# Performance work log

Measured on AMD Instinct MI355X. Metric: run time of the kernel, lower is better.

The kernel has to match this reference:

```python
import jax, jax.numpy as jnp
from jax import lax
import numpy as np

SCALE_N = 4
KERN = 5
PAD = KERN // 2
_G = np.float32([[0.003765, 0.015019, 0.023792, 0.015019, 0.003765],
                 [0.015019, 0.059912, 0.094907, 0.059912, 0.015019],
                 [0.023792, 0.094907, 0.150342, 0.094907, 0.023792],
                 [0.015019, 0.059912, 0.094907, 0.059912, 0.015019],
                 [0.003765, 0.015019, 0.023792, 0.015019, 0.003765]])
FILTER = jnp.asarray(_G)


def _lap_split(img):
    N, c, H, W = img.shape
    f = jnp.broadcast_to(FILTER, (c, 1, KERN, KERN))
    smooth = lax.conv_general_dilated(img, f, (1, 1), [(PAD, PAD), (PAD, PAD)],
                                      feature_group_count=c)
    lo = smooth[:, :, ::2, ::2]
    oph, opw = (H + 1) % 2, (W + 1) % 2
    # conv_transpose2d(stride=2, padding=PAD, output_padding) as lhs-dilated conv
    # (Gaussian kernel is symmetric, so no spatial flip needed)
    lo2 = 4.0 * lax.conv_general_dilated(
        lo, f, (1, 1),
        [(KERN - 1 - PAD, KERN - 1 - PAD + oph), (KERN - 1 - PAD, KERN - 1 - PAD + opw)],
        lhs_dilation=(2, 2), feature_group_count=c)
    hi = img - lo2
    return lo, hi


def _pyramid(img):
    levels = []
    for _ in range(SCALE_N):
        img, hi = _lap_split(img)
        levels.append(hi)
    levels.append(img)
    return levels


def _sample_points(img, xs, ys):
    # bilinear grid_sample, align_corners=False, zero padding.
    # img: (N,C,H,W); xs, ys: (P,) normalized coords in [-1,1]. -> (N,C,P)
    N, C, H, W = img.shape
    fx = ((xs + 1.0) * W - 1.0) * 0.5
    fy = ((ys + 1.0) * H - 1.0) * 0.5
    x0 = jnp.floor(fx)
    y0 = jnp.floor(fy)
    wx = fx - x0
    wy = fy - y0
    x0i = x0.astype(jnp.int32)
    y0i = y0.astype(jnp.int32)
    out = jnp.zeros((N, C, xs.shape[0]), img.dtype)
    corners = [(0, 0, (1 - wx) * (1 - wy)), (1, 0, wx * (1 - wy)),
               (0, 1, (1 - wx) * wy), (1, 1, wx * wy)]
    for dx, dy, w in corners:
        xc = x0i + dx
        yc = y0i + dy
        valid = (xc >= 0) & (xc < W) & (yc >= 0) & (yc < H)
        xcc = jnp.clip(xc, 0, W - 1)
        ycc = jnp.clip(yc, 0, H - 1)
        vals = img[:, :, ycc, xcc]  # (N,C,P) gather
        out = out + vals * (w * valid)[None, None, :]
    return out


def setup_inputs() -> dict:
    key = jax.random.key(0)
    k1, k2, k3 = jax.random.split(key, 3)
    N, c, H, W = 64, 32, 128, 128
    outdims = 4096
    m = SCALE_N + 1
    x = jax.random.normal(k1, (N, c, H, W), dtype=jnp.float32)
    grid = jax.random.uniform(k2, (1, outdims, 1, 2), minval=-0.1, maxval=0.1,
                              dtype=jnp.float32)
    features = (jnp.full((1, m * c, 1, outdims), 1.0 / c, jnp.float32)
                + 0.01 * jax.random.normal(k3, (1, m * c, 1, outdims), jnp.float32))
    bias = jnp.zeros((outdims,), jnp.float32)
    return {"x": x, "grid": grid, "features": features, "bias": bias}


def reference(x, grid, features, bias):
    N, c, H, W = x.shape
    m = SCALE_N + 1
    outdims = grid.shape[1]
    g = jnp.clip(grid, -1.0, 1.0)
    xs = g[0, :, 0, 0]  # width coord
    ys = g[0, :, 0, 1]  # height coord
    levels = _pyramid(x)
    pools = [_sample_points(lv, xs, ys) for lv in levels]  # each (N,c,P)
    y = jnp.concatenate(pools, axis=1)  # (N, m*c, P)
    feat = features.reshape(1, m * c, outdims)
    y = (y * feat).sum(axis=1)  # (N, P)
    return y + bias
```

## Files before the change

### kernel.cpp

```cpp
#include <hip/hip_runtime.h>


#define P1 66
#define P2 34
#define P3 18
#define P4 10
#define OFF_LO1 0
#define OFF_LO2 4224
#define OFF_LO3 5312
#define OFF_LO4 5600
#define SLOT    5680

#define G_A 0.0613609f
#define G_B 0.2447700f
#define G_C 0.3877386f

static __device__ __forceinline__ float clampf(float v, float lo, float hi) {
    return fminf(fmaxf(v, lo), hi);
}
static __device__ __forceinline__ int imin(int a, int b) { return a < b ? a : b; }
static __device__ __forceinline__ int imax(int a, int b) { return a > b ? a : b; }

__global__ void init_out_kernel(const float* __restrict__ bias, float* __restrict__ y) {
    int i = blockIdx.x * blockDim.x + threadIdx.x;
    y[i] = bias[i & 4095];
}

__global__ void weights_kernel(const float* __restrict__ grid, float* __restrict__ ws) {
    int out = blockIdx.x * blockDim.x + threadIdx.x;
    if (out >= 4096) return;
    float xs = clampf(grid[2 * out + 0], -1.f, 1.f);
    float ys = clampf(grid[2 * out + 1], -1.f, 1.f);
    float rec[88];

    float fx = (xs + 1.f) * 64.f - 0.5f;
    float fy = (ys + 1.f) * 64.f - 0.5f;
    float x0f = floorf(fx), y0f = floorf(fy);
    int x0 = (int)x0f, y0 = (int)y0f;
    float wx = fx - x0f, wy = fy - y0f;
    float ux0 = (x0 >= 0)      ? (1.f - wx) : 0.f;
    float ux1 = (x0 + 1 < 128) ? wx         : 0.f;
    float uy0 = (y0 >= 0)      ? (1.f - wy) : 0.f;
    float uy1 = (y0 + 1 < 128) ? wy         : 0.f;
    int cx0 = imax(x0, 0), cx1 = imin(x0 + 1, 127);
    int cy0 = imax(y0, 0), cy1 = imin(y0 + 1, 127);
    rec[0] = ux0 * uy0; rec[1] = ux1 * uy0; rec[2] = ux0 * uy1; rec[3] = ux1 * uy1;
    rec[4] = __int_as_float(cy0 * 128 + cx0);
    rec[5] = __int_as_float(cy0 * 128 + cx1);
    rec[6] = __int_as_float(cy1 * 128 + cx0);
    rec[7] = __int_as_float(cy1 * 128 + cx1);

    int   x0p = x0, y0p = y0;
    float ux0p = ux0, ux1p = ux1, uy0p = uy0, uy1p = uy1;

    const int offs[4]    = {OFF_LO1, OFF_LO2, OFF_LO3, OFF_LO4};
    const int strides[4] = {P1, P2, P3, P4};

    for (int j = 1; j <= 4; ++j) {
        const int Wj = 128 >> j, Pj = strides[j - 1], off = offs[j - 1];

        int qx; float a0, a1, a2;
        if (x0p & 1) { qx = (x0p - 1) >> 1;
            a0 = G_B * ux0p + G_A * ux1p; a1 = G_B * ux0p + G_C * ux1p; a2 = G_A * ux1p; }
        else         { qx = (x0p >> 1) - 1;
            a0 = G_A * ux0p; a1 = G_C * ux0p + G_B * ux1p; a2 = G_A * ux0p + G_B * ux1p; }
        int qy; float e0, e1, e2;
        if (y0p & 1) { qy = (y0p - 1) >> 1;
            e0 = G_B * uy0p + G_A * uy1p; e1 = G_B * uy0p + G_C * uy1p; e2 = G_A * uy1p; }
        else         { qy = (y0p >> 1) - 1;
            e0 = G_A * uy0p; e1 = G_C * uy0p + G_B * uy1p; e2 = G_A * uy0p + G_B * uy1p; }

        float half = (float)(Wj >> 1);
        float fxj = (xs + 1.f) * half - 0.5f;
        float fyj = (ys + 1.f) * half - 0.5f;
        float x0jf = floorf(fxj), y0jf = floorf(fyj);
        int x0j = (int)x0jf, y0j = (int)y0jf;
        float wxj = fxj - x0jf, wyj = fyj - y0jf;
        float ux0j = (x0j >= 0)     ? (1.f - wxj) : 0.f;
        float ux1j = (x0j + 1 < Wj) ? wxj         : 0.f;
        float uy0j = (y0j >= 0)     ? (1.f - wyj) : 0.f;
        float uy1j = (y0j + 1 < Wj) ? wyj         : 0.f;

        int bxb = qx & ~1;
        bxb = imin(imax(bxb, 0), Wj - 4);

        float* L = rec + 8 + (j - 1) * 20;
#pragma unroll
        for (int t = 0; t < 4; ++t) {
            int col = bxb + t;
            int s = col - qx;
            float av = (s == 0) ? a0 : (s == 1) ? a1 : (s == 2) ? a2 : 0.f;
            if (s < 0 || s > 2) av = 0.f;
            int sb = col - x0j;
            float bv = (sb == 0) ? ux0j : (sb == 1) ? ux1j : 0.f;
            L[t] = av;
            L[4 + t] = bv;
        }
#pragma unroll
        for (int t = 0; t < 3; ++t) {
            int row = qy + t;
            bool v = (row >= 0) && (row < Wj);
            float av = (t == 0) ? e0 : (t == 1) ? e1 : e2;
            L[8 + t] = v ? av : 0.f;
            int sb = row - y0j;
            L[12 + t] = (sb == 0) ? uy0j : (sb == 1) ? uy1j : 0.f;
            int rc = imin(imax(row, 0), Wj - 1);
            L[16 + t] = __int_as_float(off + rc * Pj + bxb);
        }
        L[11] = 0.f; L[15] = 0.f; L[19] = 0.f;

        x0p = x0j; y0p = y0j;
        ux0p = ux0j; ux1p = ux1j; uy0p = uy0j; uy1p = uy1j;
    }

    float4* W = (float4*)ws;
#pragma unroll
    for (int m = 0; m < 22; ++m) {
        W[m * 4096 + out] = make_float4(rec[4 * m], rec[4 * m + 1],
                                        rec[4 * m + 2], rec[4 * m + 3]);
    }
}

static __device__ __forceinline__ float down_pt_lds(const float* s, int stride, int S,
                                                    int i, int j) {
    const float g1[5] = {G_A, G_B, G_C, G_B, G_A};
    int by = 2 * i - 2, bx = 2 * j - 2;
    float acc = 0.f;
    if (by >= 0 && by + 4 < S && bx >= 0 && bx + 4 < S) {
#pragma unroll
        for (int dy = 0; dy < 5; ++dy) {
            const float* r = s + (by + dy) * stride + bx;
            acc += g1[dy] * (G_A * (r[0] + r[4]) + G_B * (r[1] + r[3]) + G_C * r[2]);
        }
    } else {
#pragma unroll
        for (int dy = 0; dy < 5; ++dy) {
            int yy = by + dy;
            if ((unsigned)yy < (unsigned)S) {
#pragma unroll
                for (int dx = 0; dx < 5; ++dx) {
                    int xx = bx + dx;
                    if ((unsigned)xx < (unsigned)S)
                        acc += g1[dy] * g1[dx] * s[yy * stride + xx];
                }
            }
        }
    }
    return acc;
}

__global__ __launch_bounds__(256, 3) void pyr_sample_kernel(
    const float* __restrict__ x, const float* __restrict__ wrec,
    const float* __restrict__ feat, float* __restrict__ y)
{
    __shared__ float s_lo[SLOT];
    const int tid = threadIdx.x;
    const int n   = blockIdx.x >> 5;
    const int c   = blockIdx.x & 31;
    const float* img = x + ((size_t)(n * 32 + c) << 14);

    const float g1[5] = {G_A, G_B, G_C, G_B, G_A};

    for (int r = tid; r < 1024; r += 256) {
        int i = r >> 4, j0 = (r & 15) << 2;
        int by = 2 * i - 2, bx = 2 * j0 - 2;
        float acc[4] = {0.f, 0.f, 0.f, 0.f};
        if (i >= 1 && i <= 62 && j0 >= 4 && j0 <= 56) {
#pragma unroll
            for (int dy = 0; dy < 5; ++dy) {
                const float* row = img + (by + dy) * 128 + bx;
                float v[11];
#pragma unroll
                for (int t = 0; t < 11; ++t) v[t] = row[t];
                float g = g1[dy];
#pragma unroll
                for (int jj = 0; jj < 4; ++jj) {
                    float h = G_A * (v[2 * jj] + v[2 * jj + 4]) +
                              G_B * (v[2 * jj + 1] + v[2 * jj + 3]) +
                              G_C * v[2 * jj + 2];
                    acc[jj] += g * h;
                }
            }
        } else {
#pragma unroll
            for (int dy = 0; dy < 5; ++dy) {
                int yy = by + dy;
                if ((unsigned)yy < 128u) {
#pragma unroll
                    for (int t = 0; t < 11; ++t) {
                        int xx = bx + t;
                        if ((unsigned)xx < 128u) {
                            float v = img[yy * 128 + xx];
#pragma unroll
                            for (int jj = 0; jj < 4; ++jj) {
                                int dx = t - 2 * jj;
                                if (dx >= 0 && dx <= 4) acc[jj] += g1[dy] * g1[dx] * v;
                            }
                        }
                    }
                }
            }
        }
        int base = OFF_LO1 + i * P1 + j0;
        *(float2*)&s_lo[base]     = make_float2(acc[0], acc[1]);
        *(float2*)&s_lo[base + 2] = make_float2(acc[2], acc[3]);
    }
    __syncthreads();

    for (int p = tid; p < 1024; p += 256) {
        int i = p >> 5, j = p & 31;
        s_lo[OFF_LO2 + i * P2 + j] = down_pt_lds(s_lo + OFF_LO1, P1, 64, i, j);
    }
    __syncthreads();

    {
        int i = tid >> 4, j = tid & 15;
        s_lo[OFF_LO3 + i * P3 + j] = down_pt_lds(s_lo + OFF_LO2, P2, 32, i, j);
    }
    __syncthreads();

    if (tid < 64) {
        int i = tid >> 3, j = tid & 7;
        s_lo[OFF_LO4 + i * P4 + j] = down_pt_lds(s_lo + OFF_LO3, P3, 16, i, j);
    }
    __syncthreads();

    const float4* W = (const float4*)wrec;
    float* yrow = y + ((size_t)n << 12);
    for (int out = tid; out < 4096; out += 256) {
        float4 w0 = W[out];
        float4 t1 = W[4096 + out];
        int o00 = __float_as_int(t1.x), o01 = __float_as_int(t1.y);
        int o10 = __float_as_int(t1.z), o11 = __float_as_int(t1.w);

        float f_prev = feat[((size_t)c << 12) + out];
        float v0 = w0.x * img[o00] + w0.y * img[o01] + w0.z * img[o10] + w0.w * img[o11];
        float acc = f_prev * v0;

#pragma unroll
        for (int j = 1; j <= 4; ++j) {
            const int mb = (2 + 5 * (j - 1)) * 4096 + out;
            const float4 axw = W[mb];
            const float4 bxw = W[mb + 4096];
            const float4 ayw = W[mb + 2 * 4096];
            const float4 byw = W[mb + 3 * 4096];
            const float4 rrf = W[mb + 4 * 4096];
            int r0 = __float_as_int(rrf.x);
            int r1 = __float_as_int(rrf.y);
            int r2 = __float_as_int(rrf.z);

            float f_cur = feat[((size_t)(j * 32 + c) << 12) + out];

            float2 p0a = *(const float2*)&s_lo[r0];
            float2 p0b = *(const float2*)&s_lo[r0 + 2];
            float2 p1a = *(const float2*)&s_lo[r1];
            float2 p1b = *(const float2*)&s_lo[r1 + 2];
            float2 p2a = *(const float2*)&s_lo[r2];
            float2 p2b = *(const float2*)&s_lo[r2 + 2];
            float ra0 = axw.x * p0a.x + axw.y * p0a.y + axw.z * p0b.x + axw.w * p0b.y;
            float ra1 = axw.x * p1a.x + axw.y * p1a.y + axw.z * p1b.x + axw.w * p1b.y;
            float ra2 = axw.x * p2a.x + axw.y * p2a.y + axw.z * p2b.x + axw.w * p2b.y;
            float rb0 = bxw.x * p0a.x + bxw.y * p0a.y + bxw.z * p0b.x + bxw.w * p0b.y;
            float rb1 = bxw.x * p1a.x + bxw.y * p1a.y + bxw.z * p1b.x + bxw.w * p1b.y;
            float rb2 = bxw.x * p2a.x + bxw.y * p2a.y + bxw.z * p2b.x + bxw.w * p2b.y;
            float sa = ayw.x * ra0 + ayw.y * ra1 + ayw.z * ra2;
            float sb = byw.x * rb0 + byw.y * rb1 + byw.z * rb2;
            acc += f_cur * sb - 4.f * f_prev * sa;
            f_prev = f_cur;
        }
        atomicAdd(&yrow[out], acc);
    }
}

extern "C" void kernel_launch(void* const* d_in, const int* in_sizes, int n_in,
                              void* d_out, int out_size, void* d_ws, size_t ws_size,
                              hipStream_t stream) {
    (void)in_sizes; (void)n_in; (void)ws_size;
    const float* x    = (const float*)d_in[0];
    const float* grid = (const float*)d_in[1];
    const float* feat = (const float*)d_in[2];
    const float* bias = (const float*)d_in[3];
    float* y  = (float*)d_out;
    float* ws = (float*)d_ws;

    weights_kernel<<<16, 256, 0, stream>>>(grid, ws);
    init_out_kernel<<<out_size / 256, 256, 0, stream>>>(bias, y);
    pyr_sample_kernel<<<2048, 256, 0, stream>>>(x, ws, feat, y);
}
```

Before: 403.7 us.

## Split pyramid build and sampling into two kernels, replacing atomics with block reduction

The fused per-(n,c) kernel becomes two kernels. The first builds the low-pass pyramid and writes it to workspace. The second tiles over (n, 64 outputs), stages the sampling weights in LDS, loops over channels, and reduces with a shared-memory sum instead of global atomicAdd. This removes the atomic contention and the bias-init kernel, and reuses the weight records across channels. In exchange the pyramid makes an extra round trip through global memory and pyramid taps are read from global instead of LDS. A fused fallback path remains for when the workspace is too small.

```diff
diff --git a/kernel.cpp b/kernel.cpp
--- a/kernel.cpp
+++ b/kernel.cpp
@@ -14,6 +14,10 @@
 #define G_A 0.0613609f
 #define G_B 0.2447700f
 #define G_C 0.3877386f
+
+#define W4COUNT (22 * 4096)
+#define PYR_OFF_FLOATS (W4COUNT * 4)
+#define WS_NEED ((size_t)PYR_OFF_FLOATS * 4 + (size_t)2048 * SLOT * 4)
 
 static __device__ __forceinline__ float clampf(float v, float lo, float hi) {
     return fminf(fmaxf(v, lo), hi);
@@ -115,10 +119,9 @@
 
     float4* W = (float4*)ws;
 #pragma unroll
-    for (int m = 0; m < 22; ++m) {
+    for (int m = 0; m < 22; ++m)
         W[m * 4096 + out] = make_float4(rec[4 * m], rec[4 * m + 1],
                                         rec[4 * m + 2], rec[4 * m + 3]);
-    }
 }
 
 static __device__ __forceinline__ float down_pt_lds(const float* s, int stride, int S,
@@ -149,16 +152,7 @@
     return acc;
 }
 
-__global__ __launch_bounds__(256, 3) void pyr_sample_kernel(
-    const float* __restrict__ x, const float* __restrict__ wrec,
-    const float* __restrict__ feat, float* __restrict__ y)
-{
-    __shared__ float s_lo[SLOT];
-    const int tid = threadIdx.x;
-    const int n   = blockIdx.x >> 5;
-    const int c   = blockIdx.x & 31;
-    const float* img = x + ((size_t)(n * 32 + c) << 14);
-
+static __device__ void build_pyramid(const float* __restrict__ img, float* s_lo, int tid) {
     const float g1[5] = {G_A, G_B, G_C, G_B, G_A};
 
     for (int r = tid; r < 1024; r += 256) {
@@ -224,6 +218,113 @@
         s_lo[OFF_LO4 + i * P4 + j] = down_pt_lds(s_lo + OFF_LO3, P3, 16, i, j);
     }
     __syncthreads();
+}
+
+__global__ __launch_bounds__(256, 3) void pyr_build_kernel(
+    const float* __restrict__ x, float* __restrict__ pyr)
+{
+    __shared__ __align__(16) float s_lo[SLOT];
+    const int tid = threadIdx.x;
+    const float* img = x + ((size_t)blockIdx.x << 14);
+    build_pyramid(img, s_lo, tid);
+    float4* dst = (float4*)(pyr + (size_t)blockIdx.x * SLOT);
+    const float4* src = (const float4*)s_lo;
+    for (int i = tid; i < SLOT / 4; i += 256) dst[i] = src[i];
+}
+
+__global__ __launch_bounds__(256, 3) void sample_kernel(
+    const float* __restrict__ x, const float* __restrict__ wrec,
+    const float* __restrict__ pyr, const float* __restrict__ feat,
+    const float* __restrict__ bias, float* __restrict__ y)
+{
+    __shared__ __align__(16) float4 Wl[22 * 64];
+    __shared__ float red[4][64];
+    const int tid = threadIdx.x;
+    const int n   = blockIdx.x >> 6;
+    const int o0  = (blockIdx.x & 63) << 6;
+
+    const float4* Wg = (const float4*)wrec;
+    for (int i = tid; i < 22 * 64; i += 256)
+        Wl[i] = Wg[(i >> 6) * 4096 + o0 + (i & 63)];
+    __syncthreads();
+
+    const int lane = tid & 63, q = tid >> 6;
+    const int out  = o0 + lane;
+    const float* xn = x + ((size_t)n << 19);
+    const float* pn = pyr + (size_t)(n << 5) * SLOT;
+
+    float4 w0 = Wl[lane];
+    float4 t1 = Wl[64 + lane];
+    int o00 = __float_as_int(t1.x), o01 = __float_as_int(t1.y);
+    int o10 = __float_as_int(t1.z), o11 = __float_as_int(t1.w);
+
+    float acc = 0.f;
+    float fprev[8];
+#pragma unroll 4
+    for (int i = 0; i < 8; ++i) {
+        const int c = q * 8 + i;
+        const float* img = xn + ((size_t)c << 14);
+        float f = feat[((size_t)c << 12) + out];
+        float v0 = w0.x * img[o00] + w0.y * img[o01] +
+                   w0.z * img[o10] + w0.w * img[o11];
+        acc += f * v0;
+        fprev[i] = f;
+    }
+
+#pragma unroll
+    for (int j = 1; j <= 4; ++j) {
+        const int mb = (2 + 5 * (j - 1)) * 64 + lane;
+        float4 axw = Wl[mb];
+        float4 bxw = Wl[mb + 64];
+        float4 ayw = Wl[mb + 128];
+        float4 byw = Wl[mb + 192];
+        float4 rrf = Wl[mb + 256];
+        int r0 = __float_as_int(rrf.x);
+        int r1 = __float_as_int(rrf.y);
+        int r2 = __float_as_int(rrf.z);
+
+#pragma unroll 4
+        for (int i = 0; i < 8; ++i) {
+            const int c = q * 8 + i;
+            const float* P = pn + (size_t)c * SLOT;
+            float2 p0a = *(const float2*)(P + r0);
+            float2 p0b = *(const float2*)(P + r0 + 2);
+            float2 p1a = *(const float2*)(P + r1);
+            float2 p1b = *(const float2*)(P + r1 + 2);
+            float2 p2a = *(const float2*)(P + r2);
+            float2 p2b = *(const float2*)(P + r2 + 2);
+            float f = feat[((size_t)(j * 32 + c) << 12) + out];
+            float ra0 = axw.x * p0a.x + axw.y * p0a.y + axw.z * p0b.x + axw.w * p0b.y;
+            float ra1 = axw.x * p1a.x + axw.y * p1a.y + axw.z * p1b.x + axw.w * p1b.y;
+            float ra2 = axw.x * p2a.x + axw.y * p2a.y + axw.z * p2b.x + axw.w * p2b.y;
+            float rb0 = bxw.x * p0a.x + bxw.y * p0a.y + bxw.z * p0b.x + bxw.w * p0b.y;
+            float rb1 = bxw.x * p1a.x + bxw.y * p1a.y + bxw.z * p1b.x + bxw.w * p1b.y;
+            float rb2 = bxw.x * p2a.x + bxw.y * p2a.y + bxw.z * p2b.x + bxw.w * p2b.y;
+            float sa = ayw.x * ra0 + ayw.y * ra1 + ayw.z * ra2;
+            float sb = byw.x * rb0 + byw.y * rb1 + byw.z * rb2;
+            acc += f * sb - 4.f * fprev[i] * sa;
+            fprev[i] = f;
+        }
+    }
+
+    red[q][lane] = acc;
+    __syncthreads();
+    if (tid < 64) {
+        float s = red[0][tid] + red[1][tid] + red[2][tid] + red[3][tid];
+        y[((size_t)n << 12) + o0 + tid] = s + bias[o0 + tid];
+    }
+}
+
+__global__ __launch_bounds__(256, 3) void fused_fallback_kernel(
+    const float* __restrict__ x, const float* __restrict__ wrec,
+    const float* __restrict__ feat, float* __restrict__ y)
+{
+    __shared__ __align__(16) float s_lo[SLOT];
+    const int tid = threadIdx.x;
+    const int n   = blockIdx.x >> 5;
+    const int c   = blockIdx.x & 31;
+    const float* img = x + ((size_t)(n * 32 + c) << 14);
+    build_pyramid(img, s_lo, tid);
 
     const float4* W = (const float4*)wrec;
     float* yrow = y + ((size_t)n << 12);
@@ -248,9 +349,7 @@
             int r0 = __float_as_int(rrf.x);
             int r1 = __float_as_int(rrf.y);
             int r2 = __float_as_int(rrf.z);
-
             float f_cur = feat[((size_t)(j * 32 + c) << 12) + out];
-
             float2 p0a = *(const float2*)&s_lo[r0];
             float2 p0b = *(const float2*)&s_lo[r0 + 2];
             float2 p1a = *(const float2*)&s_lo[r1];
@@ -275,7 +374,7 @@
 extern "C" void kernel_launch(void* const* d_in, const int* in_sizes, int n_in,
                               void* d_out, int out_size, void* d_ws, size_t ws_size,
                               hipStream_t stream) {
-    (void)in_sizes; (void)n_in; (void)ws_size;
+    (void)in_sizes; (void)n_in;
     const float* x    = (const float*)d_in[0];
     const float* grid = (const float*)d_in[1];
     const float* feat = (const float*)d_in[2];
@@ -284,6 +383,12 @@
     float* ws = (float*)d_ws;
 
     weights_kernel<<<16, 256, 0, stream>>>(grid, ws);
-    init_out_kernel<<<out_size / 256, 256, 0, stream>>>(bias, y);
-    pyr_sample_kernel<<<2048, 256, 0, stream>>>(x, ws, feat, y);
-}
+    if (ws_size >= WS_NEED) {
+        float* pyr = ws + PYR_OFF_FLOATS;
+        pyr_build_kernel<<<2048, 256, 0, stream>>>(x, pyr);
+        sample_kernel<<<4096, 256, 0, stream>>>(x, ws, pyr, feat, bias, y);
+    } else {
+        init_out_kernel<<<out_size / 256, 256, 0, stream>>>(bias, y);
+        fused_fallback_kernel<<<2048, 256, 0, stream>>>(x, ws, feat, y);
+    }
+}
```

After: 450.3 us. +11.6%, slower.

## Pack sampling weight records into fp16 weights and 16-bit indices; vectorize level-1 loads

Applied to the files above, without the earlier changes.

Sampling weights are stored as packed half-precision pairs and the LDS/image indices as 16-bit pairs, which shrinks the per-output weight table each block streams from global memory. The level-1 downsampling now loads each input row with four aligned float4 reads instead of eleven scalar loads. The aim is less memory traffic in the gather loop at the cost of unpack instructions and reduced weight precision, which may affect accuracy tolerance.

```diff
diff --git a/kernel.cpp b/kernel.cpp
--- a/kernel.cpp
+++ b/kernel.cpp
@@ -1,4 +1,5 @@
 #include <hip/hip_runtime.h>
+#include <hip/hip_fp16.h>
 
 
 #define P1 66
@@ -15,11 +16,27 @@
 #define G_B 0.2447700f
 #define G_C 0.3877386f
 
+#define T_FOFF 16384
+
 static __device__ __forceinline__ float clampf(float v, float lo, float hi) {
     return fminf(fmaxf(v, lo), hi);
 }
 static __device__ __forceinline__ int imin(int a, int b) { return a < b ? a : b; }
 static __device__ __forceinline__ int imax(int a, int b) { return a > b ? a : b; }
+
+static __device__ __forceinline__ unsigned int pack_h2(float a, float b) {
+    __half ha = __float2half_rn(a), hb = __float2half_rn(b);
+    unsigned short ua = *(unsigned short*)&ha, ub = *(unsigned short*)&hb;
+    return (unsigned int)ua | ((unsigned int)ub << 16);
+}
+static __device__ __forceinline__ unsigned int pack_u2(int a, int b) {
+    return (unsigned int)(a & 0xffff) | ((unsigned int)b << 16);
+}
+static __device__ __forceinline__ float2 uph2(unsigned int u) {
+    unsigned short lo = (unsigned short)(u & 0xffff), hi = (unsigned short)(u >> 16);
+    __half hl = *(__half*)&lo, hh = *(__half*)&hi;
+    return make_float2(__half2float(hl), __half2float(hh));
+}
 
 __global__ void init_out_kernel(const float* __restrict__ bias, float* __restrict__ y) {
     int i = blockIdx.x * blockDim.x + threadIdx.x;
@@ -31,7 +48,9 @@
     if (out >= 4096) return;
     float xs = clampf(grid[2 * out + 0], -1.f, 1.f);
     float ys = clampf(grid[2 * out + 1], -1.f, 1.f);
-    float rec[88];
+
+    uint4* L0 = (uint4*)ws;
+    uint2* T  = (uint2*)(ws + T_FOFF);
 
     float fx = (xs + 1.f) * 64.f - 0.5f;
     float fy = (ys + 1.f) * 64.f - 0.5f;
@@ -44,11 +63,10 @@
     float uy1 = (y0 + 1 < 128) ? wy         : 0.f;
     int cx0 = imax(x0, 0), cx1 = imin(x0 + 1, 127);
     int cy0 = imax(y0, 0), cy1 = imin(y0 + 1, 127);
-    rec[0] = ux0 * uy0; rec[1] = ux1 * uy0; rec[2] = ux0 * uy1; rec[3] = ux1 * uy1;
-    rec[4] = __int_as_float(cy0 * 128 + cx0);
-    rec[5] = __int_as_float(cy0 * 128 + cx1);
-    rec[6] = __int_as_float(cy1 * 128 + cx0);
-    rec[7] = __int_as_float(cy1 * 128 + cx1);
+    L0[out] = make_uint4(pack_h2(ux0 * uy0, ux1 * uy0),
+                         pack_h2(ux0 * uy1, ux1 * uy1),
+                         pack_u2(cy0 * 128 + cx0, cy0 * 128 + cx1),
+                         pack_u2(cy1 * 128 + cx0, cy1 * 128 + cx1));
 
     int   x0p = x0, y0p = y0;
     float ux0p = ux0, ux1p = ux1, uy0p = uy0, uy1p = uy1;
@@ -84,7 +102,8 @@
         int bxb = qx & ~1;
         bxb = imin(imax(bxb, 0), Wj - 4);
 
-        float* L = rec + 8 + (j - 1) * 20;
+        float axv[4], bxv[4], ayv[3], byv[3];
+        int rv[3];
 #pragma unroll
         for (int t = 0; t < 4; ++t) {
             int col = bxb + t;
@@ -93,31 +112,30 @@
             if (s < 0 || s > 2) av = 0.f;
             int sb = col - x0j;
             float bv = (sb == 0) ? ux0j : (sb == 1) ? ux1j : 0.f;
-            L[t] = av;
-            L[4 + t] = bv;
+            axv[t] = av;
+            bxv[t] = bv;
         }
 #pragma unroll
         for (int t = 0; t < 3; ++t) {
             int row = qy + t;
             bool v = (row >= 0) && (row < Wj);
             float av = (t == 0) ? e0 : (t == 1) ? e1 : e2;
-            L[8 + t] = v ? av : 0.f;
+            ayv[t] = v ? av : 0.f;
             int sb = row - y0j;
-            L[12 + t] = (sb == 0) ? uy0j : (sb == 1) ? uy1j : 0.f;
+            byv[t] = (sb == 0) ? uy0j : (sb == 1) ? uy1j : 0.f;
             int rc = imin(imax(row, 0), Wj - 1);
-            L[16 + t] = __int_as_float(off + rc * Pj + bxb);
-        }
-        L[11] = 0.f; L[15] = 0.f; L[19] = 0.f;
+            rv[t] = off + rc * Pj + bxb;
+        }
+
+        int tb = (j - 1) * 5 * 4096 + out;
+        T[tb]            = make_uint2(pack_h2(axv[0], axv[1]), pack_h2(axv[2], axv[3]));
+        T[tb + 4096]     = make_uint2(pack_h2(bxv[0], bxv[1]), pack_h2(bxv[2], bxv[3]));
+        T[tb + 2 * 4096] = make_uint2(pack_h2(ayv[0], ayv[1]), pack_h2(ayv[2], 0.f));
+        T[tb + 3 * 4096] = make_uint2(pack_h2(byv[0], byv[1]), pack_h2(byv[2], 0.f));
+        T[tb + 4 * 4096] = make_uint2(pack_u2(rv[0], rv[1]), pack_u2(rv[2], 0));
 
         x0p = x0j; y0p = y0j;
         ux0p = ux0j; ux1p = ux1j; uy0p = uy0j; uy1p = uy1j;
-    }
-
-    float4* W = (float4*)ws;
-#pragma unroll
-    for (int m = 0; m < 22; ++m) {
-        W[m * 4096 + out] = make_float4(rec[4 * m], rec[4 * m + 1],
-                                        rec[4 * m + 2], rec[4 * m + 3]);
     }
 }
 
@@ -153,7 +171,7 @@
     const float* __restrict__ x, const float* __restrict__ wrec,
     const float* __restrict__ feat, float* __restrict__ y)
 {
-    __shared__ float s_lo[SLOT];
+    __shared__ __align__(16) float s_lo[SLOT];
     const int tid = threadIdx.x;
     const int n   = blockIdx.x >> 5;
     const int c   = blockIdx.x & 31;
@@ -163,25 +181,28 @@
 
     for (int r = tid; r < 1024; r += 256) {
         int i = r >> 4, j0 = (r & 15) << 2;
-        int by = 2 * i - 2, bx = 2 * j0 - 2;
+        int by = 2 * i - 2;
         float acc[4] = {0.f, 0.f, 0.f, 0.f};
         if (i >= 1 && i <= 62 && j0 >= 4 && j0 <= 56) {
+            const int a = 2 * j0 - 4;
 #pragma unroll
             for (int dy = 0; dy < 5; ++dy) {
-                const float* row = img + (by + dy) * 128 + bx;
-                float v[11];
-#pragma unroll
-                for (int t = 0; t < 11; ++t) v[t] = row[t];
+                const float* rp = img + (by + dy) * 128 + a;
+                float4 q0 = *(const float4*)(rp);
+                float4 q1 = *(const float4*)(rp + 4);
+                float4 q2 = *(const float4*)(rp + 8);
+                float4 q3 = *(const float4*)(rp + 12);
+                float s2 = q0.z, s3 = q0.w, s4 = q1.x, s5 = q1.y, s6 = q1.z,
+                      s7 = q1.w, s8 = q2.x, s9 = q2.y, s10 = q2.z, s11 = q2.w,
+                      s12 = q3.x;
                 float g = g1[dy];
-#pragma unroll
-                for (int jj = 0; jj < 4; ++jj) {
-                    float h = G_A * (v[2 * jj] + v[2 * jj + 4]) +
-                              G_B * (v[2 * jj + 1] + v[2 * jj + 3]) +
-                              G_C * v[2 * jj + 2];
-                    acc[jj] += g * h;
-                }
+                acc[0] += g * (G_A * (s2 + s6)  + G_B * (s3 + s5)  + G_C * s4);
+                acc[1] += g * (G_A * (s4 + s8)  + G_B * (s5 + s7)  + G_C * s6);
+                acc[2] += g * (G_A * (s6 + s10) + G_B * (s7 + s9)  + G_C * s8);
+                acc[3] += g * (G_A * (s8 + s12) + G_B * (s9 + s11) + G_C * s10);
             }
         } else {
+            int bx = 2 * j0 - 2;
 #pragma unroll
             for (int dy = 0; dy < 5; ++dy) {
                 int yy = by + dy;
@@ -225,29 +246,32 @@
     }
     __syncthreads();
 
-    const float4* W = (const float4*)wrec;
+    const uint4* L0 = (const uint4*)wrec;
+    const uint2* T  = (const uint2*)(wrec + T_FOFF);
     float* yrow = y + ((size_t)n << 12);
     for (int out = tid; out < 4096; out += 256) {
-        float4 w0 = W[out];
-        float4 t1 = W[4096 + out];
-        int o00 = __float_as_int(t1.x), o01 = __float_as_int(t1.y);
-        int o10 = __float_as_int(t1.z), o11 = __float_as_int(t1.w);
+        uint4 h0 = L0[out];
+        float2 wA = uph2(h0.x), wB = uph2(h0.y);
+        int o00 = (int)(h0.z & 0xffff), o01 = (int)(h0.z >> 16);
+        int o10 = (int)(h0.w & 0xffff), o11 = (int)(h0.w >> 16);
 
         float f_prev = feat[((size_t)c << 12) + out];
-        float v0 = w0.x * img[o00] + w0.y * img[o01] + w0.z * img[o10] + w0.w * img[o11];
+        float v0 = wA.x * img[o00] + wA.y * img[o01] + wB.x * img[o10] + wB.y * img[o11];
         float acc = f_prev * v0;
 
 #pragma unroll
         for (int j = 1; j <= 4; ++j) {
-            const int mb = (2 + 5 * (j - 1)) * 4096 + out;
-            const float4 axw = W[mb];
-            const float4 bxw = W[mb + 4096];
-            const float4 ayw = W[mb + 2 * 4096];
-            const float4 byw = W[mb + 3 * 4096];
-            const float4 rrf = W[mb + 4 * 4096];
-            int r0 = __float_as_int(rrf.x);
-            int r1 = __float_as_int(rrf.y);
-            int r2 = __float_as_int(rrf.z);
+            const int tb = (j - 1) * 5 * 4096 + out;
+            uint2 uAX = T[tb];
+            uint2 uBX = T[tb + 4096];
+            uint2 uAY = T[tb + 2 * 4096];
+            uint2 uBY = T[tb + 3 * 4096];
+            uint2 uR  = T[tb + 4 * 4096];
+            float2 ax01 = uph2(uAX.x), ax23 = uph2(uAX.y);
+            float2 bx01 = uph2(uBX.x), bx23 = uph2(uBX.y);
+            float2 ay01 = uph2(uAY.x); float ay2 = uph2(uAY.y).x;
+            float2 by01 = uph2(uBY.x); float by2 = uph2(uBY.y).x;
+            int r0 = (int)(uR.x & 0xffff), r1 = (int)(uR.x >> 16), r2 = (int)(uR.y & 0xffff);
 
             float f_cur = feat[((size_t)(j * 32 + c) << 12) + out];
 
@@ -257,14 +281,14 @@
             float2 p1b = *(const float2*)&s_lo[r1 + 2];
             float2 p2a = *(const float2*)&s_lo[r2];
             float2 p2b = *(const float2*)&s_lo[r2 + 2];
-            float ra0 = axw.x * p0a.x + axw.y * p0a.y + axw.z * p0b.x + axw.w * p0b.y;
-            float ra1 = axw.x * p1a.x + axw.y * p1a.y + axw.z * p1b.x + axw.w * p1b.y;
-            float ra2 = axw.x * p2a.x + axw.y * p2a.y + axw.z * p2b.x + axw.w * p2b.y;
-            float rb0 = bxw.x * p0a.x + bxw.y * p0a.y + bxw.z * p0b.x + bxw.w * p0b.y;
-            float rb1 = bxw.x * p1a.x + bxw.y * p1a.y + bxw.z * p1b.x + bxw.w * p1b.y;
-            float rb2 = bxw.x * p2a.x + bxw.y * p2a.y + bxw.z * p2b.x + bxw.w * p2b.y;
-            float sa = ayw.x * ra0 + ayw.y * ra1 + ayw.z * ra2;
-            float sb = byw.x * rb0 + byw.y * rb1 + byw.z * rb2;
+            float ra0 = ax01.x * p0a.x + ax01.y * p0a.y + ax23.x * p0b.x + ax23.y * p0b.y;
+            float ra1 = ax01.x * p1a.x + ax01.y * p1a.y + ax23.x * p1b.x + ax23.y * p1b.y;
+            float ra2 = ax01.x * p2a.x + ax01.y * p2a.y + ax23.x * p2b.x + ax23.y * p2b.y;
+            float rb0 = bx01.x * p0a.x + bx01.y * p0a.y + bx23.x * p0b.x + bx23.y * p0b.y;
+            float rb1 = bx01.x * p1a.x + bx01.y * p1a.y + bx23.x * p1b.x + bx23.y * p1b.y;
+            float rb2 = bx01.x * p2a.x + bx01.y * p2a.y + bx23.x * p2b.x + bx23.y * p2b.y;
+            float sa = ay01.x * ra0 + ay01.y * ra1 + ay2 * ra2;
+            float sb = by01.x * rb0 + by01.y * rb1 + by2 * rb2;
             acc += f_cur * sb - 4.f * f_prev * sa;
             f_prev = f_cur;
         }
```

New measurement: 384.3 us. 1.05x faster.
